# Performance work log

Hardware: AMD Instinct MI355X
Metric: run time of the kernel (lower is better)

Reference implementation:

```python
import jax, jax.numpy as jnp
import numpy as np

N_HEADS = 16
THETA = 10000.0

def rotate_half(x):
    x1, x2 = jnp.split(x, 2, axis=-1)
    return jnp.concatenate((-x2, x1), axis=-1)

def setup_inputs() -> dict:
    key = jax.random.key(0)
    k1, k2, k3 = jax.random.split(key, 3)
    B, T, C = 4, 2048, 2048
    x = jax.random.normal(k1, (B, T, C), dtype=jnp.float32)
    # torch Linear weights: y = x @ W.T
    wqkv = jax.random.normal(k2, (3 * C, C), dtype=jnp.float32) * (1.0 / np.sqrt(C))
    w_out = jax.random.normal(k3, (C, C), dtype=jnp.float32) * (1.0 / np.sqrt(C))
    return {"x": x, "wqkv": wqkv, "w_out": w_out}

def reference(x, wqkv, w_out):
    B, T, C = x.shape
    H = N_HEADS
    hd = C // H
    scale = 1.0 / np.sqrt(hd)

    qkv = x @ wqkv.T                               # [B, T, 3C]
    q, k, v = jnp.split(qkv, 3, axis=-1)
    q = q.reshape(B, T, H, hd).transpose(0, 2, 1, 3)  # [B, H, T, hd]
    k = k.reshape(B, T, H, hd).transpose(0, 2, 1, 3)
    v = v.reshape(B, T, H, hd).transpose(0, 2, 1, 3)

    # rotary embedding (kv_len == T, no cache)
    inv_freq = 1.0 / (THETA ** (jnp.arange(0, hd, 2, dtype=jnp.float32) / hd))
    t = jnp.arange(T, dtype=jnp.float32)
    freqs = jnp.einsum("i,j->ij", t, inv_freq)     # [T, hd/2]
    emb = jnp.concatenate((freqs, freqs), axis=-1) # [T, hd]
    cos = jnp.cos(emb)[None, None, :, :]
    sin = jnp.sin(emb)[None, None, :, :]
    q = q * cos + rotate_half(q) * sin
    k = k * cos + rotate_half(k) * sin

    scores = jnp.einsum("bhqd,bhkd->bhqk", q, k) * scale
    causal = jnp.triu(jnp.ones((T, T), dtype=bool), k=1)
    scores = jnp.where(causal[None, None], -jnp.inf, scores)
    attn = jax.nn.softmax(scores, axis=-1)
    out = jnp.einsum("bhqk,bhkd->bhqd", attn, v)   # [B, H, T, hd]
    out = out.transpose(0, 2, 1, 3).reshape(B, T, C)
    output = out @ w_out.T
    return (output, k, v)
```

## Files before the change

### kernel.cpp

```cpp
#include <hip/hip_runtime.h>

#define B_ 4
#define T_ 2048
#define C_ 2048
#define H_ 16
#define HD_ 128
#define BT_ (B_*T_)
#define N3_ (3*C_)

typedef unsigned short u16;
typedef unsigned int u32;
using short8 = __attribute__((ext_vector_type(8))) short;
using f32x4  = __attribute__((ext_vector_type(4))) float;

__device__ __forceinline__ u16 f2bf(float f) {
  union { float f; u32 u; } v; v.f = f;
  u32 r = v.u + 0x7FFFu + ((v.u >> 16) & 1u);
  return (u16)(r >> 16);
}
__device__ __forceinline__ float bf2f(u16 u) {
  union { u32 u; float f; } v; v.u = ((u32)u) << 16;
  return v.f;
}
__device__ __forceinline__ void gload_lds16(const void* g, void* l) {
  __builtin_amdgcn_global_load_lds((const __attribute__((address_space(1))) void*)g,
                                   (__attribute__((address_space(3))) void*)l, 16, 0, 0);
}

__global__ __launch_bounds__(256) void cast_f2b_kernel(const float* __restrict__ in,
                                                       u16* __restrict__ out, int n4) {
  int i = blockIdx.x * 256 + threadIdx.x;
  if (i >= n4) return;
  float4 v = ((const float4*)in)[i];
  ushort4 o;
  o.x = f2bf(v.x); o.y = f2bf(v.y); o.z = f2bf(v.z); o.w = f2bf(v.w);
  ((ushort4*)out)[i] = o;
}

__global__ __launch_bounds__(256) void rope_table_kernel(float* __restrict__ cosb,
                                                         float* __restrict__ sinb) {
  int i = blockIdx.x * 256 + threadIdx.x;
  int t = i >> 6, d = i & 63;
  float inv = powf(10000.0f, -(float)d / 64.0f);
  float ang = (float)t * inv;
  cosb[i] = cosf(ang);
  sinb[i] = sinf(ang);
}

__global__ __launch_bounds__(256) void rope_apply_kernel(const u16* __restrict__ qkv,
    const float* __restrict__ cosb, const float* __restrict__ sinb,
    u16* __restrict__ qb, u16* __restrict__ kbb,
    float* __restrict__ kout, float* __restrict__ vout) {
  int gid = blockIdx.x * 256 + threadIdx.x;
  int d = gid & 63;
  int h = (gid >> 6) & 15;
  int t = (gid >> 10) & 2047;
  int b = gid >> 21;
  const u16* row = qkv + (size_t)(b * T_ + t) * N3_;
  int base = h * HD_ + d;
  const float SCALE = 0.08838834764831845f;
  float q0 = bf2f(row[base]);
  float q1 = bf2f(row[base + 64]);
  float k0 = bf2f(row[C_ + base]);
  float k1 = bf2f(row[C_ + base + 64]);
  float v0 = bf2f(row[2*C_ + base]);
  float v1 = bf2f(row[2*C_ + base + 64]);
  float c = cosb[t * 64 + d], s = sinb[t * 64 + d];
  size_t o = ((size_t)((b * H_ + h) * T_ + t)) * HD_ + d;
  qb[o]        = f2bf((q0 * c - q1 * s) * SCALE);
  qb[o + 64]   = f2bf((q1 * c + q0 * s) * SCALE);
  float kr0 = k0 * c - k1 * s;
  float kr1 = k1 * c + k0 * s;
  kout[o]      = kr0;
  kout[o + 64] = kr1;
  kbb[o]       = f2bf(kr0);
  kbb[o + 64]  = f2bf(kr1);
  vout[o]      = v0;
  vout[o + 64] = v1;
}

__global__ __launch_bounds__(256) void vt_kernel(const u16* __restrict__ qkvb,
                                                 u16* __restrict__ vtb) {
  __shared__ u16 tile[64][72];
  int bid = blockIdx.x;
  int dh = bid & 1, tt = (bid >> 1) & 31, bh = bid >> 6;
  int b = bh >> 4, h = bh & 15;
  int tid = threadIdx.x;
  int tr = tid >> 2, tc = tid & 3;
  const u16* src = qkvb + (size_t)(b*T_ + tt*64 + tr) * N3_ + 2*C_ + h*HD_ + dh*64 + tc*16;
  short8 v0 = *(const short8*)src;
  short8 v1 = *(const short8*)(src + 8);
  #pragma unroll
  for (int j = 0; j < 8; ++j) {
    tile[tr][tc*16 + j]     = (u16)v0[j];
    tile[tr][tc*16 + 8 + j] = (u16)v1[j];
  }
  __syncthreads();
  int dr = tid >> 2, c2 = tid & 3;
  short8 o0, o1;
  #pragma unroll
  for (int j = 0; j < 8; ++j) {
    o0[j] = (short)tile[c2*16 + j][dr];
    o1[j] = (short)tile[c2*16 + 8 + j][dr];
  }
  u16* dst = vtb + ((size_t)bh * HD_ + dh*64 + dr) * T_ + tt*64 + c2*16;
  *(short8*)dst = o0;
  *(short8*)(dst + 8) = o1;
}

template<int OUT_BF16>
__global__ __launch_bounds__(512, 2) void gemm3p_kernel(const u16* __restrict__ A,
    const u16* __restrict__ Bw, void* __restrict__ Cout, int M, int N, int K, int ntx) {
  extern __shared__ u16 ldsx[];
  int lin = blockIdx.x;
  int x = lin & 7, q = lin >> 3;
  int j = q & 31, rr = q >> 5;
  int rid = rr * 8 + x;
  int rgn = ntx >> 2;
  int rmr = rid / rgn, rnr = rid - rmr * rgn;
  int mtile = rmr * 8 + (j >> 2);
  int ntile = rnr * 4 + (j & 3);
  int tid = threadIdx.x, w = tid >> 6, l = tid & 63;
  int lr = l & 15, lg = l >> 4;
  int wr = w >> 2, wc = w & 3;
  const u16* Abase = A + (size_t)mtile * 256 * K;
  const u16* Bbase = Bw + (size_t)ntile * 256 * K;

  int srow[2], scol[2], sdst[2];
  #pragma unroll
  for (int jj = 0; jj < 2; ++jj) {
    int s = jj*512 + tid;
    srow[jj] = (s >> 6)*8 + (s & 7);
    scol[jj] = ((s >> 3) & 7) * 8;
    sdst[jj] = s * 8;
  }
  int arow[8], brow[4];
  #pragma unroll
  for (int mi = 0; mi < 8; ++mi) {
    int rho = mi*16 + lr;
    arow[mi] = (rho >> 3)*512 + (rho & 7)*8 + lg*64;
  }
  #pragma unroll
  for (int nj = 0; nj < 4; ++nj) {
    int rho = (wc & 1)*64 + nj*16 + lr;
    brow[nj] = (rho >> 3)*512 + (rho & 7)*8 + lg*64;
  }
  const int haOff = (2 + wr) * 8192;
  const int hbOff = (wc >> 1) * 8192;

  auto stageB = [&](int Tp) {
    u16* dst = ldsx + (Tp & 1) * 32768;
    const u16* g = Bbase + Tp * 64;
    #pragma unroll
    for (int jj = 0; jj < 2; ++jj)
      gload_lds16(g + (size_t)srow[jj] * K + scol[jj], dst + sdst[jj]);
    #pragma unroll
    for (int jj = 0; jj < 2; ++jj)
      gload_lds16(g + (size_t)(128 + srow[jj]) * K + scol[jj], dst + 8192 + sdst[jj]);
  };
  auto stageA = [&](int Tp) {
    u16* dst = ldsx + (Tp & 1) * 32768 + 16384;
    const u16* g = Abase + Tp * 64;
    #pragma unroll
    for (int jj = 0; jj < 2; ++jj)
      gload_lds16(g + (size_t)srow[jj] * K + scol[jj], dst + sdst[jj]);
    #pragma unroll
    for (int jj = 0; jj < 2; ++jj)
      gload_lds16(g + (size_t)(128 + srow[jj]) * K + scol[jj], dst + 8192 + sdst[jj]);
  };

  short8 am03[4][2], am47[4][2], bn01[2][2], bn23[2][2];
  auto readQ0 = [&](int T) {
    const u16* base = ldsx + (T & 1) * 32768;
    #pragma unroll
    for (int i = 0; i < 4; ++i)
      #pragma unroll
      for (int kk = 0; kk < 2; ++kk)
        am03[i][kk] = *(const short8*)(base + haOff + arow[i] + kk*256);
    #pragma unroll
    for (int jj = 0; jj < 2; ++jj)
      #pragma unroll
      for (int kk = 0; kk < 2; ++kk)
        bn01[jj][kk] = *(const short8*)(base + hbOff + brow[jj] + kk*256);
  };

  f32x4 acc[8][4];
  #pragma unroll
  for (int mi = 0; mi < 8; ++mi)
    #pragma unroll
    for (int n = 0; n < 4; ++n) acc[mi][n] = (f32x4){0.f,0.f,0.f,0.f};

  const int NT = K >> 6;
  stageB(0); stageA(0); stageB(1); stageA(1);
  asm volatile("s_waitcnt vmcnt(8)" ::: "memory");
  __builtin_amdgcn_sched_barrier(0);
  __builtin_amdgcn_s_barrier();
  readQ0(0);

  for (int T = 0; T < NT; ++T) {
    const u16* base = ldsx + (T & 1) * 32768;
    bool stg = (T + 2) < NT;
    #pragma unroll
    for (int jj = 0; jj < 2; ++jj)
      #pragma unroll
      for (int kk = 0; kk < 2; ++kk)
        bn23[jj][kk] = *(const short8*)(base + hbOff + brow[2+jj] + kk*256);
    __builtin_amdgcn_s_barrier();
    __builtin_amdgcn_s_setprio(1);
    #pragma unroll
    for (int i = 0; i < 4; ++i)
      #pragma unroll
      for (int jj = 0; jj < 2; ++jj)
        #pragma unroll
        for (int kk = 0; kk < 2; ++kk)
          acc[i][jj] = __builtin_amdgcn_mfma_f32_16x16x32_bf16(am03[i][kk], bn01[jj][kk], acc[i][jj], 0, 0, 0);
    __builtin_amdgcn_s_setprio(0);
    __builtin_amdgcn_s_barrier();
    if (stg) stageB(T + 2);
    #pragma unroll
    for (int i = 0; i < 4; ++i)
      #pragma unroll
      for (int kk = 0; kk < 2; ++kk)
        am47[i][kk] = *(const short8*)(base + haOff + arow[4+i] + kk*256);
    __builtin_amdgcn_s_barrier();
    __builtin_amdgcn_s_setprio(1);
    #pragma unroll
    for (int i = 0; i < 4; ++i)
      #pragma unroll
      for (int jj = 0; jj < 2; ++jj)
        #pragma unroll
        for (int kk = 0; kk < 2; ++kk)
          acc[i][2+jj] = __builtin_amdgcn_mfma_f32_16x16x32_bf16(am03[i][kk], bn23[jj][kk], acc[i][2+jj], 0, 0, 0);
    __builtin_amdgcn_s_setprio(0);
    __builtin_amdgcn_s_barrier();
    if (stg) {
      stageA(T + 2);
      asm volatile("s_waitcnt vmcnt(8)" ::: "memory");
    } else {
      asm volatile("s_waitcnt vmcnt(0)" ::: "memory");
    }
    __builtin_amdgcn_sched_barrier(0);
    __builtin_amdgcn_s_barrier();
    __builtin_amdgcn_s_setprio(1);
    #pragma unroll
    for (int i = 0; i < 4; ++i)
      #pragma unroll
      for (int jj = 0; jj < 2; ++jj)
        #pragma unroll
        for (int kk = 0; kk < 2; ++kk)
          acc[4+i][2+jj] = __builtin_amdgcn_mfma_f32_16x16x32_bf16(am47[i][kk], bn23[jj][kk], acc[4+i][2+jj], 0, 0, 0);
    #pragma unroll
    for (int i = 0; i < 4; ++i)
      #pragma unroll
      for (int jj = 0; jj < 2; ++jj)
        #pragma unroll
        for (int kk = 0; kk < 2; ++kk)
          acc[4+i][jj] = __builtin_amdgcn_mfma_f32_16x16x32_bf16(am47[i][kk], bn01[jj][kk], acc[4+i][jj], 0, 0, 0);
    __builtin_amdgcn_s_setprio(0);
    if (T + 1 < NT) readQ0(T + 1);
    __builtin_amdgcn_s_barrier();
  }
  #pragma unroll
  for (int mi = 0; mi < 8; ++mi)
    #pragma unroll
    for (int n = 0; n < 4; ++n)
      #pragma unroll
      for (int r = 0; r < 4; ++r) {
        int grow = mtile*256 + wr*128 + mi*16 + lg*4 + r;
        int gcol = ntile*256 + wc*64 + n*16 + lr;
        float v = acc[mi][n][r];
        if (OUT_BF16) ((u16*)Cout)[(size_t)grow * N + gcol] = f2bf(v);
        else          ((float*)Cout)[(size_t)grow * N + gcol] = v;
      }
}

struct TileSt {
  short8 aq[4];
  f32x4 oacc[8];
  float m_run;
  float l_run;
};

__device__ __forceinline__ void stage_kv(const u16* kpl, const u16* vpl, int kt,
                                         u16* Kd, u16* Vd, int w, int l) {
  const u16* kTile = kpl + (size_t)kt * 64 * HD_;
  int ktOff = kt * 64;
  #pragma unroll
  for (int j = 0; j < 4; ++j) {
    int s = (j*4 + w)*64 + l;
    int g = s ^ ((s >> 4) & 7);
    gload_lds16(kTile + (g >> 4)*HD_ + (g & 15)*8, (char*)Kd + (j*4 + w)*1024);
    int g2 = s ^ ((s >> 3) & 7);
    gload_lds16(vpl + (size_t)(g2 >> 3)*T_ + ktOff + (g2 & 7)*8, (char*)Vd + (j*4 + w)*1024);
  }
}

__device__ __forceinline__ void attn_tile(TileSt& st, const u16* Kl, const u16* Vl,
                                          char* Pw, bool diag, int lr, int lg, int w) {
  f32x4 s2[4];
  #pragma unroll
  for (int ct = 0; ct < 4; ++ct) s2[ct] = (f32x4){0.f, 0.f, 0.f, 0.f};
  __builtin_amdgcn_s_setprio(1);
  #pragma unroll
  for (int kg = 0; kg < 4; ++kg) {
    #pragma unroll
    for (int ct = 0; ct < 4; ++ct) {
      int krow = ct*16 + lr;
      int kbyte = (krow*256 + (kg*32 + lg*8)*2) ^ ((krow & 7) << 4);
      short8 bk = *(const short8*)((const char*)Kl + kbyte);
      s2[ct] = __builtin_amdgcn_mfma_f32_16x16x32_bf16(bk, st.aq[kg], s2[ct], 0, 0, 0);
    }
  }
  __builtin_amdgcn_s_setprio(0);
  float p2[4][4];
  #pragma unroll
  for (int ct = 0; ct < 4; ++ct)
    #pragma unroll
    for (int r = 0; r < 4; ++r) {
      float sv = s2[ct][r];
      if (diag && (ct*16 + lg*4 + r) > (w*16 + lr)) sv = -INFINITY;
      p2[ct][r] = sv;
    }
  float mx = p2[0][0];
  #pragma unroll
  for (int ct = 0; ct < 4; ++ct)
    #pragma unroll
    for (int r = 0; r < 4; ++r) mx = fmaxf(mx, p2[ct][r]);
  mx = fmaxf(mx, __shfl_xor(mx, 16));
  mx = fmaxf(mx, __shfl_xor(mx, 32));
  float mn = fmaxf(st.m_run, mx);
  float fac = __expf(st.m_run - mn);
  st.m_run = mn;
  float ls = 0.f;
  #pragma unroll
  for (int ct = 0; ct < 4; ++ct)
    #pragma unroll
    for (int r = 0; r < 4; ++r) {
      float pv = __expf(p2[ct][r] - mn);
      p2[ct][r] = pv;
      ls += pv;
    }
  ls += __shfl_xor(ls, 16);
  ls += __shfl_xor(ls, 32);
  st.l_run = st.l_run * fac + ls;
  float facr[4];
  #pragma unroll
  for (int r = 0; r < 4; ++r) facr[r] = __shfl(fac, lg*4 + r);
  #pragma unroll
  for (int dt = 0; dt < 8; ++dt)
    #pragma unroll
    for (int r = 0; r < 4; ++r) st.oacc[dt][r] *= facr[r];
  #pragma unroll
  for (int ct = 0; ct < 4; ++ct) {
    u32 lo = (u32)f2bf(p2[ct][0]) | ((u32)f2bf(p2[ct][1]) << 16);
    u32 hi = (u32)f2bf(p2[ct][2]) | ((u32)f2bf(p2[ct][3]) << 16);
    int pb = (lr*128 + (ct*16 + lg*4)*2) ^ ((lr & 7) << 4);
    uint2 pk2 = {lo, hi};
    *(uint2*)(Pw + pb) = pk2;
  }
  asm volatile("s_waitcnt lgkmcnt(0)" ::: "memory");
  __builtin_amdgcn_sched_barrier(0);
  short8 pa[2];
  #pragma unroll
  for (int kk = 0; kk < 2; ++kk) {
    int pb = (lr*128 + (kk*32 + lg*8)*2) ^ ((lr & 7) << 4);
    pa[kk] = *(const short8*)(Pw + pb);
  }
  __builtin_amdgcn_s_setprio(1);
  #pragma unroll
  for (int dt = 0; dt < 8; ++dt) {
    #pragma unroll
    for (int kk = 0; kk < 2; ++kk) {
      int vrow = dt*16 + lr;
      int vbyte = (vrow*128 + (kk*32 + lg*8)*2) ^ ((vrow & 7) << 4);
      short8 bv = *(const short8*)((const char*)Vl + vbyte);
      st.oacc[dt] = __builtin_amdgcn_mfma_f32_16x16x32_bf16(pa[kk], bv, st.oacc[dt], 0, 0, 0);
    }
  }
  __builtin_amdgcn_s_setprio(0);
}

__device__ __forceinline__ void write_out(TileSt& st, u16* __restrict__ ao,
                                          int b, int h, int qbase, int lr, int lg, int w) {
  float invl[4];
  #pragma unroll
  for (int r = 0; r < 4; ++r) invl[r] = 1.0f / __shfl(st.l_run, lg*4 + r);
  #pragma unroll
  for (int dt = 0; dt < 8; ++dt)
    #pragma unroll
    for (int r = 0; r < 4; ++r) {
      int t = qbase + w*16 + lg*4 + r;
      int col = h*HD_ + dt*16 + lr;
      ao[(size_t)(b * T_ + t) * C_ + col] = f2bf(st.oacc[dt][r] * invl[r]);
    }
}

__global__ __launch_bounds__(256, 2) void attn_kernel(const u16* __restrict__ qb,
    const u16* __restrict__ kb, const u16* __restrict__ vtb, u16* __restrict__ ao) {
  __shared__ u16 Kl[2][64 * 128];
  __shared__ u16 Vl[2][128 * 64];
  __shared__ u16 Pl[4][16 * 64];
  int bid0 = blockIdx.x;
  int bid = (bid0 & 7) * 128 + (bid0 >> 3);
  int bh = bid >> 4, pr = bid & 15;
  int lo = pr, hi = 31 - pr;
  int b = bh >> 4, h = bh & 15;
  int tid = threadIdx.x, w = tid >> 6, l = tid & 63;
  int lr = l & 15, lg = l >> 4;
  const u16* qptr = qb + (size_t)bh * T_ * HD_;
  const u16* kpl  = kb + (size_t)bh * T_ * HD_;
  const u16* vpl  = vtb + (size_t)bh * HD_ * T_;
  char* Pw = (char*)&Pl[w][0];

  TileSt stL, stH;
  #pragma unroll
  for (int kg = 0; kg < 4; ++kg) {
    stL.aq[kg] = *(const short8*)(qptr + (size_t)(lo*64 + w*16 + lr) * HD_ + kg*32 + lg*8);
    stH.aq[kg] = *(const short8*)(qptr + (size_t)(hi*64 + w*16 + lr) * HD_ + kg*32 + lg*8);
  }
  #pragma unroll
  for (int dt = 0; dt < 8; ++dt) {
    stL.oacc[dt] = (f32x4){0.f, 0.f, 0.f, 0.f};
    stH.oacc[dt] = (f32x4){0.f, 0.f, 0.f, 0.f};
  }
  stL.m_run = -INFINITY; stH.m_run = -INFINITY;
  stL.l_run = 0.f;       stH.l_run = 0.f;

  stage_kv(kpl, vpl, 0, &Kl[0][0], &Vl[0][0], w, l);
  __syncthreads();
  int cur = 0;
  for (int kt = 0; kt <= hi; ++kt) {
    if (kt < hi) stage_kv(kpl, vpl, kt + 1, &Kl[cur ^ 1][0], &Vl[cur ^ 1][0], w, l);
    attn_tile(stH, &Kl[cur][0], &Vl[cur][0], Pw, kt == hi, lr, lg, w);
    if (kt <= lo) attn_tile(stL, &Kl[cur][0], &Vl[cur][0], Pw, kt == lo, lr, lg, w);
    __syncthreads();
    cur ^= 1;
  }
  write_out(stH, ao, b, h, hi*64, lr, lg, w);
  write_out(stL, ao, b, h, lo*64, lr, lg, w);
}

extern "C" void kernel_launch(void* const* d_in, const int* in_sizes, int n_in,
                              void* d_out, int out_size, void* d_ws, size_t ws_size,
                              hipStream_t stream) {
  const float* x     = (const float*)d_in[0];
  const float* wqkv  = (const float*)d_in[1];
  const float* w_out = (const float*)d_in[2];
  float* out = (float*)d_out;

  char* ws = (char*)d_ws;
  size_t off = 0;
  u16* xb    = (u16*)(ws + off); off += (size_t)BT_ * C_ * 2;
  u16* wqkvb = (u16*)(ws + off); off += (size_t)N3_ * C_ * 2;
  u16* woutb = (u16*)(ws + off); off += (size_t)C_ * C_ * 2;
  u16* qkvb  = (u16*)(ws + off); off += (size_t)BT_ * N3_ * 2;
  u16* qbf   = (u16*)(ws + off); off += (size_t)BT_ * C_ * 2;
  u16* aob   = (u16*)(ws + off); off += (size_t)BT_ * C_ * 2;
  u16* kbb   = (u16*)(ws + off); off += (size_t)BT_ * C_ * 2;
  u16* vtb   = (u16*)(ws + off); off += (size_t)BT_ * C_ * 2;
  float* cosb = (float*)(ws + off); off += (size_t)T_ * 64 * 4;
  float* sinb = (float*)(ws + off); off += (size_t)T_ * 64 * 4;

  float* kout = out + (size_t)BT_ * C_;
  float* vout = out + 2 * (size_t)BT_ * C_;

  hipFuncSetAttribute((const void*)gemm3p_kernel<1>,
                      hipFuncAttributeMaxDynamicSharedMemorySize, 131072);
  hipFuncSetAttribute((const void*)gemm3p_kernel<0>,
                      hipFuncAttributeMaxDynamicSharedMemorySize, 131072);

  cast_f2b_kernel<<<(BT_*C_/4)/256, 256, 0, stream>>>(x, xb, BT_*C_/4);
  cast_f2b_kernel<<<(N3_*C_/4)/256, 256, 0, stream>>>(wqkv, wqkvb, N3_*C_/4);
  cast_f2b_kernel<<<(C_*C_/4)/256, 256, 0, stream>>>(w_out, woutb, C_*C_/4);
  rope_table_kernel<<<(T_*64)/256, 256, 0, stream>>>(cosb, sinb);
  gemm3p_kernel<1><<<(N3_/256)*(BT_/256), 512, 131072, stream>>>(xb, wqkvb, qkvb, BT_, N3_, C_, N3_/256);
  rope_apply_kernel<<<(B_*T_*H_*64)/256, 256, 0, stream>>>(qkvb, cosb, sinb, qbf, kbb, kout, vout);
  vt_kernel<<<B_*H_*(T_/64)*2, 256, 0, stream>>>(qkvb, vtb);
  attn_kernel<<<B_*H_*16, 256, 0, stream>>>(qbf, kbb, vtb, aob);
  gemm3p_kernel<0><<<(C_/256)*(BT_/256), 512, 131072, stream>>>(aob, woutb, out, BT_, C_, C_, C_/256);
}
```

Baseline: 539.5 us.

## Switch GEMM inner loop to 32x32x16 bf16 MFMA tiles

After: 545.3 us. No clear change (+1.1%).

```diff
diff --git a/kernel.cpp b/kernel.cpp
--- a/kernel.cpp
+++ b/kernel.cpp
@@ -12,6 +12,7 @@
 typedef unsigned int u32;
 using short8 = __attribute__((ext_vector_type(8))) short;
 using f32x4  = __attribute__((ext_vector_type(4))) float;
+using f32x16 = __attribute__((ext_vector_type(16))) float;
 
 __device__ __forceinline__ u16 f2bf(float f) {
   union { float f; u32 u; } v; v.f = f;
@@ -108,8 +109,30 @@
   *(short8*)(dst + 8) = o1;
 }
 
+#define MM32(S) do { \
+  _Pragma("unroll") \
+  for (int mb_ = 0; mb_ < 4; ++mb_) \
+    _Pragma("unroll") \
+    for (int nb_ = 0; nb_ < 2; ++nb_) \
+      acc[mb_][nb_] = __builtin_amdgcn_mfma_f32_32x32x16_bf16(am##S[mb_], bn##S[nb_], acc[mb_][nb_], 0, 0, 0); \
+} while (0)
+
+#define READA(S, T, KS) do { \
+  const u16* bse_ = ldsx + (size_t)((T) & 1) * 32768; \
+  _Pragma("unroll") \
+  for (int mb_ = 0; mb_ < 4; ++mb_) \
+    am##S[mb_] = *(const short8*)(bse_ + haOff + aoff[mb_] + (KS)*128); \
+} while (0)
+
+#define READB(S, T, KS) do { \
+  const u16* bse_ = ldsx + (size_t)((T) & 1) * 32768; \
+  _Pragma("unroll") \
+  for (int nb_ = 0; nb_ < 2; ++nb_) \
+    bn##S[nb_] = *(const short8*)(bse_ + hbOff + boff[nb_] + (KS)*128); \
+} while (0)
+
 template<int OUT_BF16>
-__global__ __launch_bounds__(512, 2) void gemm3p_kernel(const u16* __restrict__ A,
+__global__ __launch_bounds__(512, 2) void gemm32_kernel(const u16* __restrict__ A,
     const u16* __restrict__ Bw, void* __restrict__ Cout, int M, int N, int K, int ntx) {
   extern __shared__ u16 ldsx[];
   int lin = blockIdx.x;
@@ -121,7 +144,7 @@
   int mtile = rmr * 8 + (j >> 2);
   int ntile = rnr * 4 + (j & 3);
   int tid = threadIdx.x, w = tid >> 6, l = tid & 63;
-  int lr = l & 15, lg = l >> 4;
+  int alo = l & 31, al5 = l >> 5;
   int wr = w >> 2, wc = w & 3;
   const u16* Abase = A + (size_t)mtile * 256 * K;
   const u16* Bbase = Bw + (size_t)ntile * 256 * K;
@@ -134,16 +157,16 @@
     scol[jj] = ((s >> 3) & 7) * 8;
     sdst[jj] = s * 8;
   }
-  int arow[8], brow[4];
-  #pragma unroll
-  for (int mi = 0; mi < 8; ++mi) {
-    int rho = mi*16 + lr;
-    arow[mi] = (rho >> 3)*512 + (rho & 7)*8 + lg*64;
-  }
-  #pragma unroll
-  for (int nj = 0; nj < 4; ++nj) {
-    int rho = (wc & 1)*64 + nj*16 + lr;
-    brow[nj] = (rho >> 3)*512 + (rho & 7)*8 + lg*64;
+  int aoff[4], boff[2];
+  #pragma unroll
+  for (int mb = 0; mb < 4; ++mb) {
+    int r = mb*32 + alo;
+    aoff[mb] = (r >> 3)*512 + (r & 7)*8 + al5*64;
+  }
+  #pragma unroll
+  for (int nb = 0; nb < 2; ++nb) {
+    int r = (wc & 1)*64 + nb*32 + alo;
+    boff[nb] = (r >> 3)*512 + (r & 7)*8 + al5*64;
   }
   const int haOff = (2 + wr) * 8192;
   const int hbOff = (wc >> 1) * 8192;
@@ -169,68 +192,41 @@
       gload_lds16(g + (size_t)(128 + srow[jj]) * K + scol[jj], dst + 8192 + sdst[jj]);
   };
 
-  short8 am03[4][2], am47[4][2], bn01[2][2], bn23[2][2];
-  auto readQ0 = [&](int T) {
-    const u16* base = ldsx + (T & 1) * 32768;
-    #pragma unroll
-    for (int i = 0; i < 4; ++i)
+  short8 am0[4], am1[4], am2[4], am3[4];
+  short8 bn0[2], bn1[2], bn2[2], bn3[2];
+  f32x16 acc[4][2];
+  #pragma unroll
+  for (int mb = 0; mb < 4; ++mb)
+    #pragma unroll
+    for (int nb = 0; nb < 2; ++nb)
       #pragma unroll
-      for (int kk = 0; kk < 2; ++kk)
-        am03[i][kk] = *(const short8*)(base + haOff + arow[i] + kk*256);
-    #pragma unroll
-    for (int jj = 0; jj < 2; ++jj)
-      #pragma unroll
-      for (int kk = 0; kk < 2; ++kk)
-        bn01[jj][kk] = *(const short8*)(base + hbOff + brow[jj] + kk*256);
-  };
-
-  f32x4 acc[8][4];
-  #pragma unroll
-  for (int mi = 0; mi < 8; ++mi)
-    #pragma unroll
-    for (int n = 0; n < 4; ++n) acc[mi][n] = (f32x4){0.f,0.f,0.f,0.f};
+      for (int rg = 0; rg < 16; ++rg) acc[mb][nb][rg] = 0.f;
 
   const int NT = K >> 6;
   stageB(0); stageA(0); stageB(1); stageA(1);
   asm volatile("s_waitcnt vmcnt(8)" ::: "memory");
   __builtin_amdgcn_sched_barrier(0);
   __builtin_amdgcn_s_barrier();
-  readQ0(0);
+  READA(0, 0, 0);
+  READB(0, 0, 0);
 
   for (int T = 0; T < NT; ++T) {
-    const u16* base = ldsx + (T & 1) * 32768;
     bool stg = (T + 2) < NT;
-    #pragma unroll
-    for (int jj = 0; jj < 2; ++jj)
-      #pragma unroll
-      for (int kk = 0; kk < 2; ++kk)
-        bn23[jj][kk] = *(const short8*)(base + hbOff + brow[2+jj] + kk*256);
+    READB(1, T, 1);
+    READB(2, T, 2);
+    READB(3, T, 3);
     __builtin_amdgcn_s_barrier();
     __builtin_amdgcn_s_setprio(1);
-    #pragma unroll
-    for (int i = 0; i < 4; ++i)
-      #pragma unroll
-      for (int jj = 0; jj < 2; ++jj)
-        #pragma unroll
-        for (int kk = 0; kk < 2; ++kk)
-          acc[i][jj] = __builtin_amdgcn_mfma_f32_16x16x32_bf16(am03[i][kk], bn01[jj][kk], acc[i][jj], 0, 0, 0);
+    MM32(0);
     __builtin_amdgcn_s_setprio(0);
     __builtin_amdgcn_s_barrier();
     if (stg) stageB(T + 2);
-    #pragma unroll
-    for (int i = 0; i < 4; ++i)
-      #pragma unroll
-      for (int kk = 0; kk < 2; ++kk)
-        am47[i][kk] = *(const short8*)(base + haOff + arow[4+i] + kk*256);
+    READA(1, T, 1);
+    READA(2, T, 2);
+    READA(3, T, 3);
     __builtin_amdgcn_s_barrier();
     __builtin_amdgcn_s_setprio(1);
-    #pragma unroll
-    for (int i = 0; i < 4; ++i)
-      #pragma unroll
-      for (int jj = 0; jj < 2; ++jj)
-        #pragma unroll
-        for (int kk = 0; kk < 2; ++kk)
-          acc[i][2+jj] = __builtin_amdgcn_mfma_f32_16x16x32_bf16(am03[i][kk], bn23[jj][kk], acc[i][2+jj], 0, 0, 0);
+    MM32(1);
     __builtin_amdgcn_s_setprio(0);
     __builtin_amdgcn_s_barrier();
     if (stg) {
@@ -242,33 +238,24 @@
     __builtin_amdgcn_sched_barrier(0);
     __builtin_amdgcn_s_barrier();
     __builtin_amdgcn_s_setprio(1);
-    #pragma unroll
-    for (int i = 0; i < 4; ++i)
+    MM32(2);
+    MM32(3);
+    __builtin_amdgcn_s_setprio(0);
+    if (T + 1 < NT) {
+      READA(0, T + 1, 0);
+      READB(0, T + 1, 0);
+    }
+    __builtin_amdgcn_s_barrier();
+  }
+  #pragma unroll
+  for (int mb = 0; mb < 4; ++mb)
+    #pragma unroll
+    for (int nb = 0; nb < 2; ++nb)
       #pragma unroll
-      for (int jj = 0; jj < 2; ++jj)
-        #pragma unroll
-        for (int kk = 0; kk < 2; ++kk)
-          acc[4+i][2+jj] = __builtin_amdgcn_mfma_f32_16x16x32_bf16(am47[i][kk], bn23[jj][kk], acc[4+i][2+jj], 0, 0, 0);
-    #pragma unroll
-    for (int i = 0; i < 4; ++i)
-      #pragma unroll
-      for (int jj = 0; jj < 2; ++jj)
-        #pragma unroll
-        for (int kk = 0; kk < 2; ++kk)
-          acc[4+i][jj] = __builtin_amdgcn_mfma_f32_16x16x32_bf16(am47[i][kk], bn01[jj][kk], acc[4+i][jj], 0, 0, 0);
-    __builtin_amdgcn_s_setprio(0);
-    if (T + 1 < NT) readQ0(T + 1);
-    __builtin_amdgcn_s_barrier();
-  }
-  #pragma unroll
-  for (int mi = 0; mi < 8; ++mi)
-    #pragma unroll
-    for (int n = 0; n < 4; ++n)
-      #pragma unroll
-      for (int r = 0; r < 4; ++r) {
-        int grow = mtile*256 + wr*128 + mi*16 + lg*4 + r;
-        int gcol = ntile*256 + wc*64 + n*16 + lr;
-        float v = acc[mi][n][r];
+      for (int rg = 0; rg < 16; ++rg) {
+        int grow = mtile*256 + wr*128 + mb*32 + (rg & 3) + 8*(rg >> 2) + 4*al5;
+        int gcol = ntile*256 + wc*64 + nb*32 + alo;
+        float v = acc[mb][nb][rg];
         if (OUT_BF16) ((u16*)Cout)[(size_t)grow * N + gcol] = f2bf(v);
         else          ((float*)Cout)[(size_t)grow * N + gcol] = v;
       }
@@ -464,18 +451,18 @@
   float* kout = out + (size_t)BT_ * C_;
   float* vout = out + 2 * (size_t)BT_ * C_;
 
-  hipFuncSetAttribute((const void*)gemm3p_kernel<1>,
+  hipFuncSetAttribute((const void*)gemm32_kernel<1>,
                       hipFuncAttributeMaxDynamicSharedMemorySize, 131072);
-  hipFuncSetAttribute((const void*)gemm3p_kernel<0>,
+  hipFuncSetAttribute((const void*)gemm32_kernel<0>,
                       hipFuncAttributeMaxDynamicSharedMemorySize, 131072);
 
   cast_f2b_kernel<<<(BT_*C_/4)/256, 256, 0, stream>>>(x, xb, BT_*C_/4);
   cast_f2b_kernel<<<(N3_*C_/4)/256, 256, 0, stream>>>(wqkv, wqkvb, N3_*C_/4);
   cast_f2b_kernel<<<(C_*C_/4)/256, 256, 0, stream>>>(w_out, woutb, C_*C_/4);
   rope_table_kernel<<<(T_*64)/256, 256, 0, stream>>>(cosb, sinb);
-  gemm3p_kernel<1><<<(N3_/256)*(BT_/256), 512, 131072, stream>>>(xb, wqkvb, qkvb, BT_, N3_, C_, N3_/256);
+  gemm32_kernel<1><<<(N3_/256)*(BT_/256), 512, 131072, stream>>>(xb, wqkvb, qkvb, BT_, N3_, C_, N3_/256);
   rope_apply_kernel<<<(B_*T_*H_*64)/256, 256, 0, stream>>>(qkvb, cosb, sinb, qbf, kbb, kout, vout);
   vt_kernel<<<B_*H_*(T_/64)*2, 256, 0, stream>>>(qkvb, vtb);
   attn_kernel<<<B_*H_*16, 256, 0, stream>>>(qbf, kbb, vtb, aob);
-  gemm3p_kernel<0><<<(C_/256)*(BT_/256), 512, 131072, stream>>>(aob, woutb, out, BT_, C_, C_, C_/256);
-}
+  gemm32_kernel<0><<<(C_/256)*(BT_/256), 512, 131072, stream>>>(aob, woutb, out, BT_, C_, C_, C_/256);
+}
```
